# Performance work log

Measured on AMD Instinct MI355X. Metric: run time of the kernel, lower is better.

Reference implementation:

```python
import jax, jax.numpy as jnp
import numpy as np

H = 4            # attention heads (HGTConv and SGFormer)
HID = 128        # hidden_dim
D = HID // H     # per-head dim in HGT
OUT = 128        # out_dim
L = 2            # number of HGT layers
NE, NA = 60000, 30000
E_EE, E_EA, E_AE = 150000, 75000, 75000


def setup_inputs() -> dict:
    ks = iter(jax.random.split(jax.random.key(0), 64))

    def nrm(shape, s=0.05):
        return jax.random.normal(next(ks), shape, dtype=jnp.float32) * s

    return {
        "x_entity": nrm((NE, HID), 1.0),
        "x_attr": nrm((NA, HID), 1.0),
        "Wkqv_ent": nrm((L, HID, 3 * HID)), "bkqv_ent": jnp.zeros((L, 3 * HID), jnp.float32),
        "Wkqv_att": nrm((L, HID, 3 * HID)), "bkqv_att": jnp.zeros((L, 3 * HID), jnp.float32),
        "Wout_ent": nrm((L, HID, HID)), "bout_ent": jnp.zeros((L, HID), jnp.float32),
        "Wout_att": nrm((L, HID, HID)), "bout_att": jnp.zeros((L, HID), jnp.float32),
        "skip_ent": jnp.ones((L,), jnp.float32), "skip_att": jnp.ones((L,), jnp.float32),
        "a_rel": nrm((L, 3, H, D, D), 0.1), "m_rel": nrm((L, 3, H, D, D), 0.1),
        "p_rel": jnp.ones((L, 3, H), jnp.float32),
        "ln_ent_g": jnp.ones((HID,), jnp.float32), "ln_ent_b": jnp.zeros((HID,), jnp.float32),
        "sg_fc_W": nrm((HID, HID)), "sg_fc_b": jnp.zeros((HID,), jnp.float32),
        "sg_ln0_g": jnp.ones((HID,), jnp.float32), "sg_ln0_b": jnp.zeros((HID,), jnp.float32),
        "sg_Wq": nrm((HID, HID * H)), "sg_bq": jnp.zeros((HID * H,), jnp.float32),
        "sg_Wk": nrm((HID, HID * H)), "sg_bk": jnp.zeros((HID * H,), jnp.float32),
        "sg_Wv": nrm((HID, HID * H)), "sg_bv": jnp.zeros((HID * H,), jnp.float32),
        "sg_ln1_g": jnp.ones((HID,), jnp.float32), "sg_ln1_b": jnp.zeros((HID,), jnp.float32),
        "proj_W1": nrm((HID, OUT)), "proj_b1": jnp.zeros((OUT,), jnp.float32),
        "proj_W2": nrm((OUT, OUT)), "proj_b2": jnp.zeros((OUT,), jnp.float32),
        "ei_ee": jax.random.randint(next(ks), (2, E_EE), 0, NE),
        "ei_ea": jnp.stack([jax.random.randint(next(ks), (E_EA,), 0, NE),
                            jax.random.randint(next(ks), (E_EA,), 0, NA)]),
        "ei_ae": jnp.stack([jax.random.randint(next(ks), (E_AE,), 0, NA),
                            jax.random.randint(next(ks), (E_AE,), 0, NE)]),
    }


def _ln(x, g, b, eps=1e-5):
    mu = x.mean(-1, keepdims=True)
    var = ((x - mu) ** 2).mean(-1, keepdims=True)
    return (x - mu) * jax.lax.rsqrt(var + eps) * g + b


def _seg_softmax(alpha, idx, n):
    # numerically stable softmax over edges grouped by destination node
    m = jax.ops.segment_max(alpha, idx, num_segments=n)
    e = jnp.exp(alpha - m[idx])
    s = jax.ops.segment_sum(e, idx, num_segments=n)
    return e / (s[idx] + 1e-16)


def _hgt_layer(x_e, x_a, Wkqv_e, bkqv_e, Wkqv_a, bkqv_a, Wout_e, bout_e,
               Wout_a, bout_a, sk_e, sk_a, a_rel, m_rel, p_rel,
               ei_ee, ei_ea, ei_ae):
    ne, na = x_e.shape[0], x_a.shape[0]
    # HeteroDictLinear producing [k|q|v], split along channels then reshape [N,H,D]
    kqv_e = (x_e @ Wkqv_e + bkqv_e).reshape(ne, 3, H, D)
    kqv_a = (x_a @ Wkqv_a + bkqv_a).reshape(na, 3, H, D)
    kd = {"e": kqv_e[:, 0], "a": kqv_a[:, 0]}
    qd = {"e": kqv_e[:, 1], "a": kqv_a[:, 1]}
    vd = {"e": kqv_e[:, 2], "a": kqv_a[:, 2]}
    nd = {"e": ne, "a": na}
    scale = 1.0 / float(np.sqrt(D))
    buf = {"e": [], "a": []}
    for t, (src, dst, ei) in enumerate([("e", "e", ei_ee), ("e", "a", ei_ea), ("a", "e", ei_ae)]):
        kt = jnp.einsum('nhd,hde->nhe', kd[src], a_rel[t])  # per-relation key transform (k_rel)
        vt = jnp.einsum('nhd,hde->nhe', vd[src], m_rel[t])  # per-relation value transform (v_rel)
        al = (qd[dst][ei[1]] * kt[ei[0]]).sum(-1) * p_rel[t] * scale  # [E,H]
        buf[dst].append((al, vt[ei[0]], ei[1]))
    outs = {}
    for dst in ("e", "a"):
        # joint softmax over ALL incoming edge types of this node type
        al = jnp.concatenate([b[0] for b in buf[dst]], 0)
        ve = jnp.concatenate([b[1] for b in buf[dst]], 0)
        ix = jnp.concatenate([b[2] for b in buf[dst]], 0)
        w = _seg_softmax(al, ix, nd[dst])
        outs[dst] = jax.ops.segment_sum(ve * w[..., None], ix,
                                        num_segments=nd[dst]).reshape(nd[dst], HID)
    o_e = jax.nn.gelu(outs["e"], approximate=False) @ Wout_e + bout_e
    o_a = jax.nn.gelu(outs["a"], approximate=False) @ Wout_a + bout_a
    g_e, g_a = jax.nn.sigmoid(sk_e), jax.nn.sigmoid(sk_a)
    return g_e * o_e + (1.0 - g_e) * x_e, g_a * o_a + (1.0 - g_a) * x_a


def reference(x_entity, x_attr, Wkqv_ent, bkqv_ent, Wkqv_att, bkqv_att,
              Wout_ent, bout_ent, Wout_att, bout_att, skip_ent, skip_att,
              a_rel, m_rel, p_rel, ln_ent_g, ln_ent_b,
              sg_fc_W, sg_fc_b, sg_ln0_g, sg_ln0_b, sg_Wq, sg_bq, sg_Wk, sg_bk,
              sg_Wv, sg_bv, sg_ln1_g, sg_ln1_b,
              proj_W1, proj_b1, proj_W2, proj_b2, ei_ee, ei_ea, ei_ae):
    h_e, h_a = x_entity, x_attr
    for l in range(L):
        h_e, h_a = _hgt_layer(h_e, h_a, Wkqv_ent[l], bkqv_ent[l], Wkqv_att[l], bkqv_att[l],
                              Wout_ent[l], bout_ent[l], Wout_att[l], bout_att[l],
                              skip_ent[l], skip_att[l], a_rel[l], m_rel[l], p_rel[l],
                              ei_ee, ei_ea, ei_ae)
        h_e = jax.nn.gelu(h_e, approximate=False)
        h_a = jax.nn.gelu(h_a, approximate=False)
    # SGFormer trans_conv: fc -> LN -> ReLU -> linear global attention -> residual -> LN
    n = h_e.shape[0]
    z0 = jax.nn.relu(_ln(h_e @ sg_fc_W + sg_fc_b, sg_ln0_g, sg_ln0_b))
    q = (z0 @ sg_Wq + sg_bq).reshape(n, H, HID)
    k = (z0 @ sg_Wk + sg_bk).reshape(n, H, HID)
    v = (z0 @ sg_Wv + sg_bv).reshape(n, H, HID)
    qs = q / jnp.linalg.norm(q)  # global Frobenius norm, as in SGFormer
    kn = k / jnp.linalg.norm(k)
    kvs = jnp.einsum('lhm,lhd->hmd', kn, v)
    num = jnp.einsum('nhm,hmd->nhd', qs, kvs) + float(n) * v
    den = jnp.einsum('nhm,hm->nh', qs, kn.sum(0))[..., None] + float(n)
    attn = (num / den).mean(1)  # mean over heads -> [n, HID]
    h_global = _ln(0.5 * attn + 0.5 * z0, sg_ln1_g, sg_ln1_b)  # residual alpha=0.5
    # alpha-blend (self.alpha = 0.1) + entity LayerNorm + projector MLP
    h_ent = _ln(0.9 * h_e + 0.1 * h_global, ln_ent_g, ln_ent_b)
    return jax.nn.relu(h_ent @ proj_W1 + proj_b1) @ proj_W2 + proj_b2
```

## Files before the change

kernel.cpp:

```cpp
#include <hip/hip_runtime.h>

#define NE 60000
#define NA 30000
#define E_EE 150000
#define E_EA 75000
#define E_AE 75000
#define SCALE 0.17677669529663689f

__device__ __forceinline__ float bf2f(unsigned short u) {
  return __uint_as_float(((unsigned)u) << 16);
}
__device__ __forceinline__ unsigned short f2bf(float f) {
  unsigned u = __float_as_uint(f);
  u = u + 0x7FFFu + ((u >> 16) & 1u);
  return (unsigned short)(u >> 16);
}
__device__ __forceinline__ float ldc(const float* p) { return *p; }
__device__ __forceinline__ float ldc(const unsigned short* p) { return bf2f(*p); }
__device__ __forceinline__ float gelu_f(float x) {
  return 0.5f * x * (1.0f + erff(x * 0.7071067811865476f));
}

__global__ __launch_bounds__(256) void wrel_k(
    const float* __restrict__ Wk_e, const float* __restrict__ Wk_a,
    const float* __restrict__ bk_e, const float* __restrict__ bk_a,
    const float* __restrict__ a_rel, const float* __restrict__ m_rel,
    float* __restrict__ Wkt, float* __restrict__ Wvt,
    float* __restrict__ bkt, float* __restrict__ bvt) {
  int t = blockIdx.x;
  int part = blockIdx.y;
  const float* W = (t < 2) ? Wk_e : Wk_a;
  const float* bb = (t < 2) ? bk_e : bk_a;
  const float* A = (part ? m_rel : a_rel) + t * 4096;
  int coff = part ? 256 : 0;
  float* Wo = (part ? Wvt : Wkt) + t * 16384;
  float* bo = (part ? bvt : bkt) + t * 128;
  __shared__ float As[4096];
  for (int u = threadIdx.x; u < 4096; u += 256) As[u] = A[u];
  __syncthreads();
  for (int u = threadIdx.x; u < 16384; u += 256) {
    int i = u >> 7, c = u & 127;
    int hh = c >> 5, e = c & 31;
    const float* wr = W + i * 384 + coff + hh * 32;
    const float* ar = As + hh * 1024 + e;
    float acc = 0.f;
#pragma unroll
    for (int d = 0; d < 32; ++d) acc = fmaf(wr[d], ar[d * 32], acc);
    Wo[u] = acc;
  }
  if (threadIdx.x < 128) {
    int c = threadIdx.x, hh = c >> 5, e = c & 31;
    const float* br = bb + coff + hh * 32;
    const float* ar = As + hh * 1024 + e;
    float acc = 0.f;
#pragma unroll
    for (int d = 0; d < 32; ++d) acc = fmaf(br[d], ar[d * 32], acc);
    bo[c] = acc;
  }
}

template <int ACT, int EPI>
__global__ __launch_bounds__(256) void gemm128_k(
    const float* __restrict__ X, int ldx,
    const float* __restrict__ W, int ldw,
    const float* __restrict__ bias, int N,
    float* __restrict__ fout, unsigned short* __restrict__ bout, int ldo,
    const float* __restrict__ skipp, float* __restrict__ ssq) {
  __shared__ float Xs[128 * 32];
  __shared__ float Ws[32 * 128];
  const int tid = threadIdx.x;
  const int ti = tid >> 4;
  const int tj = tid & 15;
  const int row0 = blockIdx.x * 128;
  const int cb = blockIdx.y * 128;
  const int c0 = cb + tj * 4;
  const int c1 = cb + 64 + tj * 4;

  float acc[8][8];
  {
    float bc[8] = {0.f, 0.f, 0.f, 0.f, 0.f, 0.f, 0.f, 0.f};
    if (bias) {
#pragma unroll
      for (int j = 0; j < 4; ++j) { bc[j] = bias[c0 + j]; bc[4 + j] = bias[c1 + j]; }
    }
#pragma unroll
    for (int i = 0; i < 8; ++i)
#pragma unroll
      for (int j = 0; j < 8; ++j) acc[i][j] = bc[j];
  }

  for (int ks = 0; ks < 128; ks += 32) {
    __syncthreads();
    for (int v = tid; v < 1024; v += 256) {
      int kq = v & 7, r = v >> 3;
      int rg = row0 + r; if (rg >= N) rg = N - 1;
      float4 x4 = *reinterpret_cast<const float4*>(X + (size_t)rg * ldx + ks + kq * 4);
      if (ACT == 1) {
        x4.x = gelu_f(x4.x); x4.y = gelu_f(x4.y);
        x4.z = gelu_f(x4.z); x4.w = gelu_f(x4.w);
      }
      *reinterpret_cast<float4*>(&Xs[r * 32 + ((kq ^ ((r >> 3) & 7)) << 2)]) = x4;
    }
    for (int v = tid; v < 1024; v += 256) {
      int cq = v & 31, k = v >> 5;
      *reinterpret_cast<float4*>(&Ws[k * 128 + cq * 4]) =
          *reinterpret_cast<const float4*>(W + (size_t)(ks + k) * ldw + cb + cq * 4);
    }
    __syncthreads();
#pragma unroll
    for (int k = 0; k < 32; k += 4) {
      float xr[8][4];
#pragma unroll
      for (int i = 0; i < 8; ++i)
        *reinterpret_cast<float4*>(xr[i]) = *reinterpret_cast<const float4*>(
            &Xs[(ti * 8 + i) * 32 + ((((k >> 2)) ^ (ti & 7)) << 2)]);
      float wr[4][8];
#pragma unroll
      for (int dk = 0; dk < 4; ++dk) {
        *reinterpret_cast<float4*>(&wr[dk][0]) =
            *reinterpret_cast<const float4*>(&Ws[(k + dk) * 128 + tj * 4]);
        *reinterpret_cast<float4*>(&wr[dk][4]) =
            *reinterpret_cast<const float4*>(&Ws[(k + dk) * 128 + 64 + tj * 4]);
      }
#pragma unroll
      for (int i = 0; i < 8; ++i)
#pragma unroll
        for (int dk = 0; dk < 4; ++dk)
#pragma unroll
          for (int j = 0; j < 8; ++j)
            acc[i][j] = fmaf(xr[i][dk], wr[dk][j], acc[i][j]);
    }
  }

  if (EPI == 0 || EPI == 1) {
#pragma unroll
    for (int i = 0; i < 8; ++i) {
      int rg = row0 + ti * 8 + i;
      if (rg < N) {
        float4 a = make_float4(acc[i][0], acc[i][1], acc[i][2], acc[i][3]);
        float4 b = make_float4(acc[i][4], acc[i][5], acc[i][6], acc[i][7]);
        if (EPI == 1) {
          a.x = fmaxf(a.x, 0.f); a.y = fmaxf(a.y, 0.f);
          a.z = fmaxf(a.z, 0.f); a.w = fmaxf(a.w, 0.f);
          b.x = fmaxf(b.x, 0.f); b.y = fmaxf(b.y, 0.f);
          b.z = fmaxf(b.z, 0.f); b.w = fmaxf(b.w, 0.f);
        }
        *reinterpret_cast<float4*>(fout + (size_t)rg * ldo + c0) = a;
        *reinterpret_cast<float4*>(fout + (size_t)rg * ldo + c1) = b;
      }
    }
  } else if (EPI == 2) {
    float loc = 0.f;
#pragma unroll
    for (int i = 0; i < 8; ++i) {
      int rg = row0 + ti * 8 + i;
      if (rg < N) {
        ushort4 s0, s1;
        s0.x = f2bf(acc[i][0]); s0.y = f2bf(acc[i][1]);
        s0.z = f2bf(acc[i][2]); s0.w = f2bf(acc[i][3]);
        s1.x = f2bf(acc[i][4]); s1.y = f2bf(acc[i][5]);
        s1.z = f2bf(acc[i][6]); s1.w = f2bf(acc[i][7]);
        *reinterpret_cast<ushort4*>(bout + (size_t)rg * ldo + c0) = s0;
        *reinterpret_cast<ushort4*>(bout + (size_t)rg * ldo + c1) = s1;
#pragma unroll
        for (int j = 0; j < 8; ++j) loc += acc[i][j] * acc[i][j];
      }
    }
    if (ssq) {
      __syncthreads();
      Xs[tid] = loc;
      __syncthreads();
      if (tid < 128) Xs[tid] += Xs[tid + 128];
      __syncthreads();
      if (tid < 64) {
        float v = Xs[tid] + Xs[tid + 64];
#pragma unroll
        for (int m = 32; m > 0; m >>= 1) v += __shfl_down(v, m, 64);
        if (tid == 0) atomicAdd(ssq, v);
      }
    }
  } else {
    float g = 1.f / (1.f + expf(-*skipp));
    float g1 = 1.f - g;
#pragma unroll
    for (int i = 0; i < 8; ++i) {
      int rg = row0 + ti * 8 + i;
      if (rg < N) {
        float4 o0 = *reinterpret_cast<const float4*>(fout + (size_t)rg * ldo + c0);
        float4 o1 = *reinterpret_cast<const float4*>(fout + (size_t)rg * ldo + c1);
        float4 a, b;
        a.x = gelu_f(g * acc[i][0] + g1 * o0.x);
        a.y = gelu_f(g * acc[i][1] + g1 * o0.y);
        a.z = gelu_f(g * acc[i][2] + g1 * o0.z);
        a.w = gelu_f(g * acc[i][3] + g1 * o0.w);
        b.x = gelu_f(g * acc[i][4] + g1 * o1.x);
        b.y = gelu_f(g * acc[i][5] + g1 * o1.y);
        b.z = gelu_f(g * acc[i][6] + g1 * o1.z);
        b.w = gelu_f(g * acc[i][7] + g1 * o1.w);
        *reinterpret_cast<float4*>(fout + (size_t)rg * ldo + c0) = a;
        *reinterpret_cast<float4*>(fout + (size_t)rg * ldo + c1) = b;
      }
    }
  }
}

template <int ACT, int EPI>
__global__ __launch_bounds__(256) void gemm64_k(
    const float* __restrict__ X, int ldx,
    const float* __restrict__ W, int ldw,
    const float* __restrict__ bias, int N,
    float* __restrict__ fout, unsigned short* __restrict__ bout, int ldo,
    const float* __restrict__ skipp, float* __restrict__ ssq) {
  __shared__ float Xs[64 * 32];
  __shared__ float Ws[32 * 128];
  const int tid = threadIdx.x;
  const int ti = tid >> 4;
  const int tj = tid & 15;
  const int row0 = blockIdx.x * 64;
  const int cb = blockIdx.y * 128;
  const int c0 = cb + tj * 4;
  const int c1 = cb + 64 + tj * 4;

  float acc[4][8];
  {
    float bc[8] = {0.f, 0.f, 0.f, 0.f, 0.f, 0.f, 0.f, 0.f};
    if (bias) {
#pragma unroll
      for (int j = 0; j < 4; ++j) { bc[j] = bias[c0 + j]; bc[4 + j] = bias[c1 + j]; }
    }
#pragma unroll
    for (int i = 0; i < 4; ++i)
#pragma unroll
      for (int j = 0; j < 8; ++j) acc[i][j] = bc[j];
  }

  for (int ks = 0; ks < 128; ks += 32) {
    __syncthreads();
    for (int v = tid; v < 512; v += 256) {
      int kq = v & 7, r = v >> 3;
      int rg = row0 + r; if (rg >= N) rg = N - 1;
      float4 x4 = *reinterpret_cast<const float4*>(X + (size_t)rg * ldx + ks + kq * 4);
      if (ACT == 1) {
        x4.x = gelu_f(x4.x); x4.y = gelu_f(x4.y);
        x4.z = gelu_f(x4.z); x4.w = gelu_f(x4.w);
      }
      *reinterpret_cast<float4*>(&Xs[r * 32 + ((kq ^ ((r >> 3) & 7)) << 2)]) = x4;
    }
    for (int v = tid; v < 1024; v += 256) {
      int cq = v & 31, k = v >> 5;
      *reinterpret_cast<float4*>(&Ws[k * 128 + cq * 4]) =
          *reinterpret_cast<const float4*>(W + (size_t)(ks + k) * ldw + cb + cq * 4);
    }
    __syncthreads();
#pragma unroll
    for (int k = 0; k < 32; k += 4) {
      float xr[4][4];
#pragma unroll
      for (int i = 0; i < 4; ++i)
        *reinterpret_cast<float4*>(xr[i]) = *reinterpret_cast<const float4*>(
            &Xs[(ti * 4 + i) * 32 + ((((k >> 2)) ^ (ti >> 1)) << 2)]);
      float wr[4][8];
#pragma unroll
      for (int dk = 0; dk < 4; ++dk) {
        *reinterpret_cast<float4*>(&wr[dk][0]) =
            *reinterpret_cast<const float4*>(&Ws[(k + dk) * 128 + tj * 4]);
        *reinterpret_cast<float4*>(&wr[dk][4]) =
            *reinterpret_cast<const float4*>(&Ws[(k + dk) * 128 + 64 + tj * 4]);
      }
#pragma unroll
      for (int i = 0; i < 4; ++i)
#pragma unroll
        for (int dk = 0; dk < 4; ++dk)
#pragma unroll
          for (int j = 0; j < 8; ++j)
            acc[i][j] = fmaf(xr[i][dk], wr[dk][j], acc[i][j]);
    }
  }

  if (EPI == 0 || EPI == 1) {
#pragma unroll
    for (int i = 0; i < 4; ++i) {
      int rg = row0 + ti * 4 + i;
      if (rg < N) {
        float4 a = make_float4(acc[i][0], acc[i][1], acc[i][2], acc[i][3]);
        float4 b = make_float4(acc[i][4], acc[i][5], acc[i][6], acc[i][7]);
        if (EPI == 1) {
          a.x = fmaxf(a.x, 0.f); a.y = fmaxf(a.y, 0.f);
          a.z = fmaxf(a.z, 0.f); a.w = fmaxf(a.w, 0.f);
          b.x = fmaxf(b.x, 0.f); b.y = fmaxf(b.y, 0.f);
          b.z = fmaxf(b.z, 0.f); b.w = fmaxf(b.w, 0.f);
        }
        *reinterpret_cast<float4*>(fout + (size_t)rg * ldo + c0) = a;
        *reinterpret_cast<float4*>(fout + (size_t)rg * ldo + c1) = b;
      }
    }
  } else if (EPI == 2) {
    float loc = 0.f;
#pragma unroll
    for (int i = 0; i < 4; ++i) {
      int rg = row0 + ti * 4 + i;
      if (rg < N) {
        ushort4 s0, s1;
        s0.x = f2bf(acc[i][0]); s0.y = f2bf(acc[i][1]);
        s0.z = f2bf(acc[i][2]); s0.w = f2bf(acc[i][3]);
        s1.x = f2bf(acc[i][4]); s1.y = f2bf(acc[i][5]);
        s1.z = f2bf(acc[i][6]); s1.w = f2bf(acc[i][7]);
        *reinterpret_cast<ushort4*>(bout + (size_t)rg * ldo + c0) = s0;
        *reinterpret_cast<ushort4*>(bout + (size_t)rg * ldo + c1) = s1;
#pragma unroll
        for (int j = 0; j < 8; ++j) loc += acc[i][j] * acc[i][j];
      }
    }
    if (ssq) {
      __syncthreads();
      Xs[tid] = loc;
      __syncthreads();
      if (tid < 128) Xs[tid] += Xs[tid + 128];
      __syncthreads();
      if (tid < 64) {
        float v = Xs[tid] + Xs[tid + 64];
#pragma unroll
        for (int m = 32; m > 0; m >>= 1) v += __shfl_down(v, m, 64);
        if (tid == 0) atomicAdd(ssq, v);
      }
    }
  } else {
    float g = 1.f / (1.f + expf(-*skipp));
    float g1 = 1.f - g;
#pragma unroll
    for (int i = 0; i < 4; ++i) {
      int rg = row0 + ti * 4 + i;
      if (rg < N) {
        float4 o0 = *reinterpret_cast<const float4*>(fout + (size_t)rg * ldo + c0);
        float4 o1 = *reinterpret_cast<const float4*>(fout + (size_t)rg * ldo + c1);
        float4 a, b;
        a.x = gelu_f(g * acc[i][0] + g1 * o0.x);
        a.y = gelu_f(g * acc[i][1] + g1 * o0.y);
        a.z = gelu_f(g * acc[i][2] + g1 * o0.z);
        a.w = gelu_f(g * acc[i][3] + g1 * o0.w);
        b.x = gelu_f(g * acc[i][4] + g1 * o1.x);
        b.y = gelu_f(g * acc[i][5] + g1 * o1.y);
        b.z = gelu_f(g * acc[i][6] + g1 * o1.z);
        b.w = gelu_f(g * acc[i][7] + g1 * o1.w);
        *reinterpret_cast<float4*>(fout + (size_t)rg * ldo + c0) = a;
        *reinterpret_cast<float4*>(fout + (size_t)rg * ldo + c1) = b;
      }
    }
  }
}

__global__ __launch_bounds__(256) void deg_k(const int* __restrict__ ei, int E,
                                             int* __restrict__ deg) {
  int i = blockIdx.x * 256 + threadIdx.x;
  if (i < E) atomicAdd(&deg[ei[E + i]], 1);
}

__global__ __launch_bounds__(1024) void scan_k(int* __restrict__ deg_cursor,
                                               int* __restrict__ rowptr, int n) {
  __shared__ int sd[1024];
  __shared__ int carry;
  int tid = threadIdx.x;
  if (tid == 0) carry = 0;
  __syncthreads();
  for (int base = 0; base < n; base += 1024) {
    int v = (base + tid < n) ? deg_cursor[base + tid] : 0;
    sd[tid] = v;
    __syncthreads();
    for (int off = 1; off < 1024; off <<= 1) {
      int t = (tid >= off) ? sd[tid - off] : 0;
      __syncthreads();
      sd[tid] += t;
      __syncthreads();
    }
    int c0 = carry;
    if (base + tid < n) {
      int excl = c0 + sd[tid] - v;
      rowptr[base + tid] = excl;
      deg_cursor[base + tid] = excl;
    }
    __syncthreads();
    if (tid == 0) carry = c0 + sd[1023];
    __syncthreads();
  }
  if (tid == 0) rowptr[n] = carry;
}

__global__ __launch_bounds__(256) void fill_k(const int* __restrict__ ei, int E,
                                              int* __restrict__ cursor,
                                              int* __restrict__ entries,
                                              int srcoff, int tag) {
  int i = blockIdx.x * 256 + threadIdx.x;
  if (i < E) {
    int pos = atomicAdd(&cursor[ei[E + i]], 1);
    entries[pos] = (ei[i] + srcoff) | (tag << 30);
  }
}

__global__ __launch_bounds__(256) void hgt_gather_k(
    const float* __restrict__ q, const unsigned short* __restrict__ ktbl,
    const unsigned short* __restrict__ vtbl, const int* __restrict__ rowptr,
    const int* __restrict__ entries, const float* __restrict__ pbase, int nd,
    float* __restrict__ out) {
  int g = blockIdx.x * 8 + (threadIdx.x >> 5);
  int dst = g >> 2, h = g & 3, c = threadIdx.x & 31;
  if (dst >= nd) return;
  int col = h * 32 + c;
  float qv = q[(size_t)dst * 128 + col];
  int i0 = rowptr[dst], i1 = rowptr[dst + 1];
  float sum = 0.f, acc = 0.f;
  for (int i = i0; i < i1; ++i) {
    int e = entries[i];
    int lin = e & 0x3FFFFFFF;
    int tag = (unsigned)e >> 30;
    float part = qv * bf2f(ktbl[(size_t)lin * 128 + col]);
#pragma unroll
    for (int m = 16; m > 0; m >>= 1) part += __shfl_xor(part, m);
    float w = expf(part * SCALE * pbase[tag * 8 + h]);
    sum += w;
    acc = fmaf(w, bf2f(vtbl[(size_t)lin * 128 + col]), acc);
  }
  out[(size_t)dst * 128 + col] = acc / (sum + 1e-16f);
}

template <typename AT, typename BT>
__global__ __launch_bounds__(128) void ln_k(const AT* __restrict__ A,
                                            const BT* __restrict__ B, float alpha,
                                            float beta, const float* __restrict__ g,
                                            const float* __restrict__ b,
                                            float* __restrict__ out, int relu) {
  int row = blockIdx.x;
  int t = threadIdx.x;
  float v = alpha * ldc(A + (size_t)row * 128 + t);
  if (B) v += beta * ldc(B + (size_t)row * 128 + t);
  float s1 = v, s2 = v * v;
#pragma unroll
  for (int m = 32; m > 0; m >>= 1) {
    s1 += __shfl_xor(s1, m, 64);
    s2 += __shfl_xor(s2, m, 64);
  }
  __shared__ float r1[2], r2[2];
  int w = t >> 6;
  if ((t & 63) == 0) { r1[w] = s1; r2[w] = s2; }
  __syncthreads();
  float S1 = r1[0] + r1[1], S2 = r2[0] + r2[1];
  float mu = S1 * (1.f / 128.f);
  float var = S2 * (1.f / 128.f) - mu * mu;
  float rr = rsqrtf(fmaxf(var, 0.f) + 1e-5f);
  float o = (v - mu) * rr * g[t] + b[t];
  if (relu) o = fmaxf(o, 0.f);
  out[(size_t)row * 128 + t] = o;
}

__global__ __launch_bounds__(256) void kvsred_k(const unsigned short* __restrict__ Kb,
                                                const unsigned short* __restrict__ Vb,
                                                float* __restrict__ part,
                                                float* __restrict__ ksum, int chunk) {
  const int h = blockIdx.y;
  const int n0 = blockIdx.x * chunk;
  const int iters = chunk >> 3;
  __shared__ float ks[8][132];
  __shared__ float vs[8][132];
  const int tid = threadIdx.x;
  const int ti = tid >> 4, tj = tid & 15;

  const int sw = tid >> 7;
  const int sni = (tid >> 4) & 7;
  const int sc = (tid & 15) << 3;
  const unsigned short* src =
      (sw ? Vb : Kb) + (size_t)(n0 + sni) * 512 + h * 128 + sc;
  float* dstrow = (sw ? &vs[0][0] : &ks[0][0]) + sni * 132 + sc;

  float acc[8][8];
#pragma unroll
  for (int i = 0; i < 8; ++i)
#pragma unroll
    for (int j = 0; j < 8; ++j) acc[i][j] = 0.f;
  float ksloc = 0.f;

  uint4 r = *reinterpret_cast<const uint4*>(src);
  for (int it = 0; it < iters; ++it) {
    __syncthreads();
    float4 lo, hi;
    lo.x = bf2f((unsigned short)(r.x & 0xffffu)); lo.y = bf2f((unsigned short)(r.x >> 16));
    lo.z = bf2f((unsigned short)(r.y & 0xffffu)); lo.w = bf2f((unsigned short)(r.y >> 16));
    hi.x = bf2f((unsigned short)(r.z & 0xffffu)); hi.y = bf2f((unsigned short)(r.z >> 16));
    hi.z = bf2f((unsigned short)(r.w & 0xffffu)); hi.w = bf2f((unsigned short)(r.w >> 16));
    *reinterpret_cast<float4*>(dstrow) = lo;
    *reinterpret_cast<float4*>(dstrow + 4) = hi;
    if (it + 1 < iters)
      r = *reinterpret_cast<const uint4*>(src + (size_t)(it + 1) * 8 * 512);
    __syncthreads();
#pragma unroll
    for (int ni = 0; ni < 8; ++ni) {
      float kk[8], vv[8];
      *reinterpret_cast<float4*>(kk) =
          *reinterpret_cast<const float4*>(&ks[ni][ti * 4]);
      *reinterpret_cast<float4*>(kk + 4) =
          *reinterpret_cast<const float4*>(&ks[ni][64 + ti * 4]);
      *reinterpret_cast<float4*>(vv) =
          *reinterpret_cast<const float4*>(&vs[ni][tj * 4]);
      *reinterpret_cast<float4*>(vv + 4) =
          *reinterpret_cast<const float4*>(&vs[ni][64 + tj * 4]);
#pragma unroll
      for (int i = 0; i < 8; ++i)
#pragma unroll
        for (int j = 0; j < 8; ++j) acc[i][j] = fmaf(kk[i], vv[j], acc[i][j]);
      if (tid < 128) ksloc += ks[ni][tid];
    }
  }
  float* pb = part + (size_t)(blockIdx.x * 4 + h) * 16384;
#pragma unroll
  for (int i = 0; i < 8; ++i) {
    int m = ti * 4 + (i & 3) + ((i >> 2) << 6);
    *reinterpret_cast<float4*>(pb + m * 128 + tj * 4) =
        make_float4(acc[i][0], acc[i][1], acc[i][2], acc[i][3]);
    *reinterpret_cast<float4*>(pb + m * 128 + 64 + tj * 4) =
        make_float4(acc[i][4], acc[i][5], acc[i][6], acc[i][7]);
  }
  if (tid < 128) atomicAdd(&ksum[h * 128 + tid], ksloc);
}

__global__ __launch_bounds__(256) void kvsfin_k(const float* __restrict__ part,
                                                float* __restrict__ kvs, int G) {
  int c = blockIdx.x * 256 + threadIdx.x;
  int hh = c >> 14, md = c & 16383;
  const float* p = part + (size_t)hh * 16384 + md;
  float s = 0.f;
#pragma unroll 4
  for (int g = 0; g < G; ++g) s += p[(size_t)g * 65536];
  kvs[c] = s;
}

__global__ __launch_bounds__(256) void sgapply_k(const unsigned short* __restrict__ Qb,
                                                 const unsigned short* __restrict__ Vb,
                                                 const float* __restrict__ kvs,
                                                 const float* __restrict__ ksum,
                                                 const float* __restrict__ ssqq,
                                                 const float* __restrict__ ssqk,
                                                 unsigned short* __restrict__ attnb,
                                                 int N) {
  __shared__ float Xs[64 * 32];
  __shared__ float Ws[32 * 128];
  __shared__ float kss[32];
  __shared__ float fsh_s;
  const int tid = threadIdx.x;
  const int ti = tid >> 4;
  const int tj = tid & 15;
  const int row0 = blockIdx.x * 64;
  if (tid == 0) fsh_s = 1.0f / (sqrtf(*ssqq) * sqrtf(*ssqk));

  float out[4][8];
#pragma unroll
  for (int i = 0; i < 4; ++i)
#pragma unroll
    for (int j = 0; j < 8; ++j) out[i][j] = 0.f;

  for (int h = 0; h < 4; ++h) {
    float acc[4][8];
    float den[4];
#pragma unroll
    for (int i = 0; i < 4; ++i) {
      den[i] = 0.f;
#pragma unroll
      for (int j = 0; j < 8; ++j) acc[i][j] = 0.f;
    }
    for (int ks = 0; ks < 128; ks += 32) {
      __syncthreads();
      for (int v = tid; v < 512; v += 256) {
        int kq = v & 7, r = v >> 3;
        int rg = row0 + r; if (rg >= N) rg = N - 1;
        ushort4 q4 = *reinterpret_cast<const ushort4*>(
            Qb + (size_t)rg * 512 + h * 128 + ks + kq * 4);
        float4 x4 = make_float4(bf2f(q4.x), bf2f(q4.y), bf2f(q4.z), bf2f(q4.w));
        *reinterpret_cast<float4*>(&Xs[r * 32 + ((kq ^ ((r >> 3) & 7)) << 2)]) = x4;
      }
      for (int v = tid; v < 1024; v += 256) {
        int cq = v & 31, k = v >> 5;
        *reinterpret_cast<float4*>(&Ws[k * 128 + cq * 4]) =
            *reinterpret_cast<const float4*>(kvs + (size_t)h * 16384 +
                                             (size_t)(ks + k) * 128 + cq * 4);
      }
      if (tid < 32) kss[tid] = ksum[h * 128 + ks + tid];
      __syncthreads();
#pragma unroll
      for (int k = 0; k < 32; k += 4) {
        float xr[4][4];
#pragma unroll
        for (int i = 0; i < 4; ++i)
          *reinterpret_cast<float4*>(xr[i]) = *reinterpret_cast<const float4*>(
              &Xs[(ti * 4 + i) * 32 + ((((k >> 2)) ^ (ti >> 1)) << 2)]);
        float wr[4][8];
        float kv[4];
#pragma unroll
        for (int dk = 0; dk < 4; ++dk) {
          *reinterpret_cast<float4*>(&wr[dk][0]) =
              *reinterpret_cast<const float4*>(&Ws[(k + dk) * 128 + tj * 4]);
          *reinterpret_cast<float4*>(&wr[dk][4]) =
              *reinterpret_cast<const float4*>(&Ws[(k + dk) * 128 + 64 + tj * 4]);
          kv[dk] = kss[k + dk];
        }
#pragma unroll
        for (int i = 0; i < 4; ++i)
#pragma unroll
          for (int dk = 0; dk < 4; ++dk) {
            den[i] = fmaf(xr[i][dk], kv[dk], den[i]);
#pragma unroll
            for (int j = 0; j < 8; ++j)
              acc[i][j] = fmaf(xr[i][dk], wr[dk][j], acc[i][j]);
          }
      }
    }
    float f = fsh_s;
#pragma unroll
    for (int i = 0; i < 4; ++i) {
      int rg = row0 + ti * 4 + i;
      if (rg < N) {
        ushort4 v0 = *reinterpret_cast<const ushort4*>(
            Vb + (size_t)rg * 512 + h * 128 + tj * 4);
        ushort4 v1 = *reinterpret_cast<const ushort4*>(
            Vb + (size_t)rg * 512 + h * 128 + 64 + tj * 4);
        float rd = 1.0f / (den[i] * f + 60000.0f);
        out[i][0] += (acc[i][0] * f + 60000.0f * bf2f(v0.x)) * rd;
        out[i][1] += (acc[i][1] * f + 60000.0f * bf2f(v0.y)) * rd;
        out[i][2] += (acc[i][2] * f + 60000.0f * bf2f(v0.z)) * rd;
        out[i][3] += (acc[i][3] * f + 60000.0f * bf2f(v0.w)) * rd;
        out[i][4] += (acc[i][4] * f + 60000.0f * bf2f(v1.x)) * rd;
        out[i][5] += (acc[i][5] * f + 60000.0f * bf2f(v1.y)) * rd;
        out[i][6] += (acc[i][6] * f + 60000.0f * bf2f(v1.z)) * rd;
        out[i][7] += (acc[i][7] * f + 60000.0f * bf2f(v1.w)) * rd;
      }
    }
  }
#pragma unroll
  for (int i = 0; i < 4; ++i) {
    int rg = row0 + ti * 4 + i;
    if (rg < N) {
      ushort4 s0, s1;
      s0.x = f2bf(0.25f * out[i][0]); s0.y = f2bf(0.25f * out[i][1]);
      s0.z = f2bf(0.25f * out[i][2]); s0.w = f2bf(0.25f * out[i][3]);
      s1.x = f2bf(0.25f * out[i][4]); s1.y = f2bf(0.25f * out[i][5]);
      s1.z = f2bf(0.25f * out[i][6]); s1.w = f2bf(0.25f * out[i][7]);
      *reinterpret_cast<ushort4*>(attnb + (size_t)rg * 128 + tj * 4) = s0;
      *reinterpret_cast<ushort4*>(attnb + (size_t)rg * 128 + 64 + tj * 4) = s1;
    }
  }
}

extern "C" void kernel_launch(void* const* d_in, const int* in_sizes, int n_in,
                              void* d_out, int out_size, void* d_ws, size_t ws_size,
                              hipStream_t stream) {
  const float* x_ent = (const float*)d_in[0];
  const float* x_att = (const float*)d_in[1];
  const float* Wkqv_e = (const float*)d_in[2];
  const float* bkqv_e = (const float*)d_in[3];
  const float* Wkqv_a = (const float*)d_in[4];
  const float* bkqv_a = (const float*)d_in[5];
  const float* Wout_e = (const float*)d_in[6];
  const float* bout_e = (const float*)d_in[7];
  const float* Wout_a = (const float*)d_in[8];
  const float* bout_a = (const float*)d_in[9];
  const float* skip_e = (const float*)d_in[10];
  const float* skip_a = (const float*)d_in[11];
  const float* a_rel = (const float*)d_in[12];
  const float* m_rel = (const float*)d_in[13];
  const float* p_rel = (const float*)d_in[14];
  const float* ln_ent_g = (const float*)d_in[15];
  const float* ln_ent_b = (const float*)d_in[16];
  const float* sg_fc_W = (const float*)d_in[17];
  const float* sg_fc_b = (const float*)d_in[18];
  const float* sg_ln0_g = (const float*)d_in[19];
  const float* sg_ln0_b = (const float*)d_in[20];
  const float* sg_Wq = (const float*)d_in[21];
  const float* sg_bq = (const float*)d_in[22];
  const float* sg_Wk = (const float*)d_in[23];
  const float* sg_bk = (const float*)d_in[24];
  const float* sg_Wv = (const float*)d_in[25];
  const float* sg_bv = (const float*)d_in[26];
  const float* sg_ln1_g = (const float*)d_in[27];
  const float* sg_ln1_b = (const float*)d_in[28];
  const float* proj_W1 = (const float*)d_in[29];
  const float* proj_b1 = (const float*)d_in[30];
  const float* proj_W2 = (const float*)d_in[31];
  const float* proj_b2 = (const float*)d_in[32];
  const int* ei_ee = (const int*)d_in[33];
  const int* ei_ea = (const int*)d_in[34];
  const int* ei_ae = (const int*)d_in[35];

  char* ws = (char*)d_ws;
  const size_t O_HE = 0;
  const size_t O_HA = 30720000;
  const size_t O_Z0 = 46080000;
  const size_t O_WKT = 76800000;
  const size_t O_WVT = 76996608;
  const size_t O_BKT = 77193216;
  const size_t O_BVT = 77194752;
  const size_t O_KVS = 77196288;
  const size_t O_RPE = 77460544;
  const size_t O_RPA = O_RPE + 240064;
  const size_t O_CUE = O_RPA + 120064;
  const size_t O_CUA = O_CUE + 240000;
  const size_t O_ENE = O_CUA + 120000;
  const size_t O_ENA = O_ENE + 900000;
  const size_t O_UN = O_ENA + 300000;
  float* q_e = (float*)(ws + O_UN);
  float* q_a = (float*)(ws + O_UN + 30720000);
  unsigned short* ktbl = (unsigned short*)(ws + O_UN + 46080000);
  unsigned short* vtbl = (unsigned short*)(ws + O_UN + 84480000);
  float* tmpf = (float*)(ws + O_UN);
  unsigned short* Vb = (unsigned short*)(ws + O_UN);
  unsigned short* KQb = (unsigned short*)(ws + O_UN + 61440000);
  unsigned short* attnb = (unsigned short*)(ws + O_HA);

  float* h_e = (float*)(ws + O_HE);
  float* h_a = (float*)(ws + O_HA);
  float* z0 = (float*)(ws + O_Z0);
  float* Wkt = (float*)(ws + O_WKT);
  float* Wvt = (float*)(ws + O_WVT);
  float* bkt = (float*)(ws + O_BKT);
  float* bvt = (float*)(ws + O_BVT);
  float* kvs = (float*)(ws + O_KVS);
  float* ksum = (float*)(ws + O_KVS + 262144);
  float* ssq_q = (float*)(ws + O_KVS + 262144 + 2048);
  float* ssq_k = ssq_q + 1;
  int* rowptr_e = (int*)(ws + O_RPE);
  int* rowptr_a = (int*)(ws + O_RPA);
  int* cursor_e = (int*)(ws + O_CUE);
  int* cursor_a = (int*)(ws + O_CUA);
  int* entries_e = (int*)(ws + O_ENE);
  int* entries_a = (int*)(ws + O_ENA);

  const int GB_E = (NE + 127) / 128;
  const int G64_E = (NE + 63) / 64;
  const int G64_A = (NA + 63) / 64;

  hipMemcpyAsync(h_e, x_ent, (size_t)NE * 128 * 4, hipMemcpyDeviceToDevice, stream);
  hipMemcpyAsync(h_a, x_att, (size_t)NA * 128 * 4, hipMemcpyDeviceToDevice, stream);

  hipMemsetAsync(ws + O_CUE, 0, 360000, stream);
  deg_k<<<(E_EE + 255) / 256, 256, 0, stream>>>(ei_ee, E_EE, cursor_e);
  deg_k<<<(E_AE + 255) / 256, 256, 0, stream>>>(ei_ae, E_AE, cursor_e);
  deg_k<<<(E_EA + 255) / 256, 256, 0, stream>>>(ei_ea, E_EA, cursor_a);
  scan_k<<<1, 1024, 0, stream>>>(cursor_e, rowptr_e, NE);
  scan_k<<<1, 1024, 0, stream>>>(cursor_a, rowptr_a, NA);
  fill_k<<<(E_EE + 255) / 256, 256, 0, stream>>>(ei_ee, E_EE, cursor_e, entries_e, 0, 0);
  fill_k<<<(E_AE + 255) / 256, 256, 0, stream>>>(ei_ae, E_AE, cursor_e, entries_e, NE, 1);
  fill_k<<<(E_EA + 255) / 256, 256, 0, stream>>>(ei_ea, E_EA, cursor_a, entries_a, 0, 0);

  for (int l = 0; l < 2; ++l) {
    const float* Wke = Wkqv_e + (size_t)l * 49152;
    const float* Wka = Wkqv_a + (size_t)l * 49152;
    const float* bke = bkqv_e + (size_t)l * 384;
    const float* bka = bkqv_a + (size_t)l * 384;

    wrel_k<<<dim3(3, 2), 256, 0, stream>>>(Wke, Wka, bke, bka,
                                           a_rel + (size_t)l * 12288,
                                           m_rel + (size_t)l * 12288, Wkt, Wvt, bkt, bvt);
    gemm64_k<0, 0><<<G64_E, 256, 0, stream>>>(h_e, 128, Wke + 128, 384, bke + 128, NE,
                                              q_e, nullptr, 128, nullptr, nullptr);
    gemm64_k<0, 0><<<G64_A, 256, 0, stream>>>(h_a, 128, Wka + 128, 384, bka + 128, NA,
                                              q_a, nullptr, 128, nullptr, nullptr);
    gemm64_k<0, 2><<<G64_E, 256, 0, stream>>>(h_e, 128, Wkt, 128, bkt, NE,
                                              nullptr, ktbl, 128, nullptr, nullptr);
    gemm64_k<0, 2><<<G64_A, 256, 0, stream>>>(h_a, 128, Wkt + 2 * 16384, 128,
                                              bkt + 2 * 128, NA, nullptr,
                                              ktbl + (size_t)NE * 128, 128, nullptr, nullptr);
    gemm64_k<0, 2><<<G64_E, 256, 0, stream>>>(h_e, 128, Wkt + 1 * 16384, 128,
                                              bkt + 1 * 128, NE, nullptr,
                                              ktbl + (size_t)90000 * 128, 128, nullptr, nullptr);
    gemm64_k<0, 2><<<G64_E, 256, 0, stream>>>(h_e, 128, Wvt, 128, bvt, NE,
                                              nullptr, vtbl, 128, nullptr, nullptr);
    gemm64_k<0, 2><<<G64_A, 256, 0, stream>>>(h_a, 128, Wvt + 2 * 16384, 128,
                                              bvt + 2 * 128, NA, nullptr,
                                              vtbl + (size_t)NE * 128, 128, nullptr, nullptr);
    gemm64_k<0, 2><<<G64_E, 256, 0, stream>>>(h_e, 128, Wvt + 1 * 16384, 128,
                                              bvt + 1 * 128, NE, nullptr,
                                              vtbl + (size_t)90000 * 128, 128, nullptr, nullptr);
    hgt_gather_k<<<30000, 256, 0, stream>>>(q_e, ktbl, vtbl, rowptr_e, entries_e,
                                            p_rel + (size_t)l * 12, NE, q_e);
    hgt_gather_k<<<15000, 256, 0, stream>>>(q_a, ktbl + (size_t)90000 * 128,
                                            vtbl + (size_t)90000 * 128, rowptr_a,
                                            entries_a, p_rel + (size_t)l * 12 + 4, NA, q_a);
    gemm64_k<1, 3><<<G64_E, 256, 0, stream>>>(q_e, 128, Wout_e + (size_t)l * 16384, 128,
                                              bout_e + (size_t)l * 128, NE, h_e, nullptr,
                                              128, skip_e + l, nullptr);
    gemm64_k<1, 3><<<G64_A, 256, 0, stream>>>(q_a, 128, Wout_a + (size_t)l * 16384, 128,
                                              bout_a + (size_t)l * 128, NA, h_a, nullptr,
                                              128, skip_a + l, nullptr);
  }

  gemm64_k<0, 0><<<G64_E, 256, 0, stream>>>(h_e, 128, sg_fc_W, 128, sg_fc_b, NE,
                                            tmpf, nullptr, 128, nullptr, nullptr);
  ln_k<float, float><<<NE, 128, 0, stream>>>(tmpf, nullptr, 1.f, 0.f, sg_ln0_g,
                                             sg_ln0_b, z0, 1);
  hipMemsetAsync(ws + O_KVS, 0, 264256, stream);
  gemm128_k<0, 2><<<dim3(GB_E, 4), 256, 0, stream>>>(z0, 128, sg_Wv, 512, sg_bv, NE,
                                                     nullptr, Vb, 512, nullptr, nullptr);
  gemm128_k<0, 2><<<dim3(GB_E, 4), 256, 0, stream>>>(z0, 128, sg_Wk, 512, sg_bk, NE,
                                                     nullptr, KQb, 512, nullptr, ssq_k);
  kvsred_k<<<dim3(100, 4), 256, 0, stream>>>(KQb, Vb, (float*)d_out, ksum, 600);
  kvsfin_k<<<256, 256, 0, stream>>>((const float*)d_out, kvs, 100);
  gemm128_k<0, 2><<<dim3(GB_E, 4), 256, 0, stream>>>(z0, 128, sg_Wq, 512, sg_bq, NE,
                                                     nullptr, KQb, 512, nullptr, ssq_q);
  sgapply_k<<<G64_E, 256, 0, stream>>>(KQb, Vb, kvs, ksum, ssq_q, ssq_k, attnb, NE);
  ln_k<unsigned short, float><<<NE, 128, 0, stream>>>(attnb, z0, 0.5f, 0.5f, sg_ln1_g,
                                                      sg_ln1_b, z0, 0);
  ln_k<float, float><<<NE, 128, 0, stream>>>(h_e, z0, 0.9f, 0.1f, ln_ent_g, ln_ent_b,
                                             h_e, 0);
  gemm64_k<0, 1><<<G64_E, 256, 0, stream>>>(h_e, 128, proj_W1, 128, proj_b1, NE,
                                            z0, nullptr, 128, nullptr, nullptr);
  gemm64_k<0, 0><<<G64_E, 256, 0, stream>>>(z0, 128, proj_W2, 128, proj_b2, NE,
                                            (float*)d_out, nullptr, 128, nullptr, nullptr);
}
```

Measured before the change: 2.025 ms.

## Use bf16 MFMA for SGFormer attention apply with transposed bf16 KV state

```diff
diff --git a/kernel.cpp b/kernel.cpp
--- a/kernel.cpp
+++ b/kernel.cpp
@@ -6,6 +6,9 @@
 #define E_EA 75000
 #define E_AE 75000
 #define SCALE 0.17677669529663689f
+
+typedef __attribute__((ext_vector_type(8))) short bf16x8;
+typedef __attribute__((ext_vector_type(4))) float f32x4;
 
 __device__ __forceinline__ float bf2f(unsigned short u) {
   return __uint_as_float(((unsigned)u) << 16);
@@ -521,127 +524,110 @@
 }
 
 __global__ __launch_bounds__(256) void kvsfin_k(const float* __restrict__ part,
-                                                float* __restrict__ kvs, int G) {
+                                                float* __restrict__ kvs,
+                                                unsigned short* __restrict__ kvsT,
+                                                int G) {
   int c = blockIdx.x * 256 + threadIdx.x;
   int hh = c >> 14, md = c & 16383;
+  int m = md >> 7, d = md & 127;
   const float* p = part + (size_t)hh * 16384 + md;
   float s = 0.f;
 #pragma unroll 4
   for (int g = 0; g < G; ++g) s += p[(size_t)g * 65536];
   kvs[c] = s;
+  kvsT[hh * 16384 + d * 128 + m] = f2bf(s);
 }
 
 __global__ __launch_bounds__(256) void sgapply_k(const unsigned short* __restrict__ Qb,
                                                  const unsigned short* __restrict__ Vb,
-                                                 const float* __restrict__ kvs,
+                                                 const unsigned short* __restrict__ kvsT,
                                                  const float* __restrict__ ksum,
                                                  const float* __restrict__ ssqq,
                                                  const float* __restrict__ ssqk,
                                                  unsigned short* __restrict__ attnb,
                                                  int N) {
-  __shared__ float Xs[64 * 32];
-  __shared__ float Ws[32 * 128];
-  __shared__ float kss[32];
+  __shared__ short Bs[16384];
+  __shared__ float den_s[64];
   __shared__ float fsh_s;
   const int tid = threadIdx.x;
-  const int ti = tid >> 4;
-  const int tj = tid & 15;
-  const int row0 = blockIdx.x * 64;
+  const int lane = tid & 63;
+  const int w = tid >> 6;
+  const int n0 = blockIdx.x * 64;
   if (tid == 0) fsh_s = 1.0f / (sqrtf(*ssqq) * sqrtf(*ssqk));
 
-  float out[4][8];
-#pragma unroll
-  for (int i = 0; i < 4; ++i)
-#pragma unroll
-    for (int j = 0; j < 8; ++j) out[i][j] = 0.f;
+  float out[8][4];
+#pragma unroll
+  for (int dt = 0; dt < 8; ++dt)
+#pragma unroll
+    for (int r = 0; r < 4; ++r) out[dt][r] = 0.f;
+
+  int arow = n0 + w * 16 + (lane & 15);
+  if (arow >= N) arow = N - 1;
+  const int kofs = (lane >> 4) * 8;
 
   for (int h = 0; h < 4; ++h) {
-    float acc[4][8];
-    float den[4];
-#pragma unroll
-    for (int i = 0; i < 4; ++i) {
-      den[i] = 0.f;
-#pragma unroll
-      for (int j = 0; j < 8; ++j) acc[i][j] = 0.f;
-    }
-    for (int ks = 0; ks < 128; ks += 32) {
-      __syncthreads();
-      for (int v = tid; v < 512; v += 256) {
-        int kq = v & 7, r = v >> 3;
-        int rg = row0 + r; if (rg >= N) rg = N - 1;
-        ushort4 q4 = *reinterpret_cast<const ushort4*>(
-            Qb + (size_t)rg * 512 + h * 128 + ks + kq * 4);
-        float4 x4 = make_float4(bf2f(q4.x), bf2f(q4.y), bf2f(q4.z), bf2f(q4.w));
-        *reinterpret_cast<float4*>(&Xs[r * 32 + ((kq ^ ((r >> 3) & 7)) << 2)]) = x4;
-      }
-      for (int v = tid; v < 1024; v += 256) {
-        int cq = v & 31, k = v >> 5;
-        *reinterpret_cast<float4*>(&Ws[k * 128 + cq * 4]) =
-            *reinterpret_cast<const float4*>(kvs + (size_t)h * 16384 +
-                                             (size_t)(ks + k) * 128 + cq * 4);
-      }
-      if (tid < 32) kss[tid] = ksum[h * 128 + ks + tid];
-      __syncthreads();
-#pragma unroll
-      for (int k = 0; k < 32; k += 4) {
-        float xr[4][4];
-#pragma unroll
-        for (int i = 0; i < 4; ++i)
-          *reinterpret_cast<float4*>(xr[i]) = *reinterpret_cast<const float4*>(
-              &Xs[(ti * 4 + i) * 32 + ((((k >> 2)) ^ (ti >> 1)) << 2)]);
-        float wr[4][8];
-        float kv[4];
-#pragma unroll
-        for (int dk = 0; dk < 4; ++dk) {
-          *reinterpret_cast<float4*>(&wr[dk][0]) =
-              *reinterpret_cast<const float4*>(&Ws[(k + dk) * 128 + tj * 4]);
-          *reinterpret_cast<float4*>(&wr[dk][4]) =
-              *reinterpret_cast<const float4*>(&Ws[(k + dk) * 128 + 64 + tj * 4]);
-          kv[dk] = kss[k + dk];
+    __syncthreads();
+    for (int s = tid; s < 2048; s += 256) {
+      int l = s & 63, dtks = s >> 6;
+      int d = (dtks >> 2) * 16 + (l & 15);
+      int kk = (dtks & 3) * 32 + (l >> 4) * 8;
+      *reinterpret_cast<bf16x8*>(&Bs[s * 8]) =
+          *reinterpret_cast<const bf16x8*>(kvsT + h * 16384 + d * 128 + kk);
+    }
+    {
+      int r = tid >> 2, seg = tid & 3;
+      int rg = n0 + r; if (rg >= N) rg = N - 1;
+      const unsigned short* qp = Qb + (size_t)rg * 512 + h * 128 + seg * 32;
+      const float* kp = ksum + h * 128 + seg * 32;
+      float p = 0.f;
+#pragma unroll
+      for (int u = 0; u < 32; u += 8) {
+        bf16x8 q8 = *reinterpret_cast<const bf16x8*>(qp + u);
+#pragma unroll
+        for (int j = 0; j < 8; ++j)
+          p = fmaf(bf2f((unsigned short)q8[j]), kp[u + j], p);
+      }
+      p += __shfl_xor(p, 1);
+      p += __shfl_xor(p, 2);
+      if (seg == 0) den_s[r] = p * fsh_s + 60000.0f;
+    }
+    __syncthreads();
+    bf16x8 afr[4];
+    {
+      const unsigned short* qrow = Qb + (size_t)arow * 512 + h * 128 + kofs;
+#pragma unroll
+      for (int ks = 0; ks < 4; ++ks)
+        afr[ks] = *reinterpret_cast<const bf16x8*>(qrow + ks * 32);
+    }
+    float f = fsh_s;
+#pragma unroll
+    for (int dt = 0; dt < 8; ++dt) {
+      f32x4 acc = {0.f, 0.f, 0.f, 0.f};
+#pragma unroll
+      for (int ks = 0; ks < 4; ++ks) {
+        bf16x8 b = *reinterpret_cast<const bf16x8*>(&Bs[((dt * 4 + ks) * 64 + lane) * 8]);
+        acc = __builtin_amdgcn_mfma_f32_16x16x32_bf16(afr[ks], b, acc, 0, 0, 0);
+      }
+      int dcol = dt * 16 + (lane & 15);
+#pragma unroll
+      for (int r = 0; r < 4; ++r) {
+        int rl = w * 16 + (lane >> 4) * 4 + r;
+        int rg = n0 + rl;
+        if (rg < N) {
+          float v = bf2f(Vb[(size_t)rg * 512 + h * 128 + dcol]);
+          float rd = 1.0f / den_s[rl];
+          out[dt][r] += (acc[r] * f + 60000.0f * v) * rd;
         }
-#pragma unroll
-        for (int i = 0; i < 4; ++i)
-#pragma unroll
-          for (int dk = 0; dk < 4; ++dk) {
-            den[i] = fmaf(xr[i][dk], kv[dk], den[i]);
-#pragma unroll
-            for (int j = 0; j < 8; ++j)
-              acc[i][j] = fmaf(xr[i][dk], wr[dk][j], acc[i][j]);
-          }
-      }
-    }
-    float f = fsh_s;
-#pragma unroll
-    for (int i = 0; i < 4; ++i) {
-      int rg = row0 + ti * 4 + i;
-      if (rg < N) {
-        ushort4 v0 = *reinterpret_cast<const ushort4*>(
-            Vb + (size_t)rg * 512 + h * 128 + tj * 4);
-        ushort4 v1 = *reinterpret_cast<const ushort4*>(
-            Vb + (size_t)rg * 512 + h * 128 + 64 + tj * 4);
-        float rd = 1.0f / (den[i] * f + 60000.0f);
-        out[i][0] += (acc[i][0] * f + 60000.0f * bf2f(v0.x)) * rd;
-        out[i][1] += (acc[i][1] * f + 60000.0f * bf2f(v0.y)) * rd;
-        out[i][2] += (acc[i][2] * f + 60000.0f * bf2f(v0.z)) * rd;
-        out[i][3] += (acc[i][3] * f + 60000.0f * bf2f(v0.w)) * rd;
-        out[i][4] += (acc[i][4] * f + 60000.0f * bf2f(v1.x)) * rd;
-        out[i][5] += (acc[i][5] * f + 60000.0f * bf2f(v1.y)) * rd;
-        out[i][6] += (acc[i][6] * f + 60000.0f * bf2f(v1.z)) * rd;
-        out[i][7] += (acc[i][7] * f + 60000.0f * bf2f(v1.w)) * rd;
-      }
-    }
-  }
-#pragma unroll
-  for (int i = 0; i < 4; ++i) {
-    int rg = row0 + ti * 4 + i;
-    if (rg < N) {
-      ushort4 s0, s1;
-      s0.x = f2bf(0.25f * out[i][0]); s0.y = f2bf(0.25f * out[i][1]);
-      s0.z = f2bf(0.25f * out[i][2]); s0.w = f2bf(0.25f * out[i][3]);
-      s1.x = f2bf(0.25f * out[i][4]); s1.y = f2bf(0.25f * out[i][5]);
-      s1.z = f2bf(0.25f * out[i][6]); s1.w = f2bf(0.25f * out[i][7]);
-      *reinterpret_cast<ushort4*>(attnb + (size_t)rg * 128 + tj * 4) = s0;
-      *reinterpret_cast<ushort4*>(attnb + (size_t)rg * 128 + 64 + tj * 4) = s1;
+      }
+    }
+  }
+#pragma unroll
+  for (int dt = 0; dt < 8; ++dt) {
+    int dcol = dt * 16 + (lane & 15);
+#pragma unroll
+    for (int r = 0; r < 4; ++r) {
+      int rg = n0 + w * 16 + (lane >> 4) * 4 + r;
+      if (rg < N) attnb[(size_t)rg * 128 + dcol] = f2bf(0.25f * out[dt][r]);
     }
   }
 }
@@ -797,11 +783,12 @@
                                                      nullptr, Vb, 512, nullptr, nullptr);
   gemm128_k<0, 2><<<dim3(GB_E, 4), 256, 0, stream>>>(z0, 128, sg_Wk, 512, sg_bk, NE,
                                                      nullptr, KQb, 512, nullptr, ssq_k);
+  unsigned short* kvsT = (unsigned short*)((char*)d_out + 26214400);
   kvsred_k<<<dim3(100, 4), 256, 0, stream>>>(KQb, Vb, (float*)d_out, ksum, 600);
-  kvsfin_k<<<256, 256, 0, stream>>>((const float*)d_out, kvs, 100);
+  kvsfin_k<<<256, 256, 0, stream>>>((const float*)d_out, kvs, kvsT, 100);
   gemm128_k<0, 2><<<dim3(GB_E, 4), 256, 0, stream>>>(z0, 128, sg_Wq, 512, sg_bq, NE,
                                                      nullptr, KQb, 512, nullptr, ssq_q);
-  sgapply_k<<<G64_E, 256, 0, stream>>>(KQb, Vb, kvs, ksum, ssq_q, ssq_k, attnb, NE);
+  sgapply_k<<<G64_E, 256, 0, stream>>>(KQb, Vb, kvsT, ksum, ssq_q, ssq_k, attnb, NE);
   ln_k<unsigned short, float><<<NE, 128, 0, stream>>>(attnb, z0, 0.5f, 0.5f, sg_ln1_g,
                                                       sg_ln1_b, z0, 0);
   ln_k<float, float><<<NE, 128, 0, stream>>>(h_e, z0, 0.9f, 0.1f, ln_ent_g, ln_ent_b,
```

Result: faster. 1.981 ms (-2.2%).
